# Optimization experiments

Measured on AMD Instinct MI355X. Metric: run time of the kernel, lower is better.

The kernel has to match this reference:

```python
import math
import jax, jax.numpy as jnp
import numpy as np

B, S, D = 8, 1024, 1024
H, DK = 16, 64
NUM_BUCKETS, MAX_DIST = 32, 128


def _relative_position_bucket(relative_position, num_buckets=NUM_BUCKETS, max_distance=MAX_DIST):
    # bidirectional=True branch of T5's bucket fn
    nb = num_buckets // 2
    n = -relative_position
    ret = (n < 0).astype(jnp.int32) * nb
    n = jnp.abs(n)
    max_exact = nb // 2
    is_small = n < max_exact
    n_safe = jnp.maximum(n, 1).astype(jnp.float32)
    val_if_large = max_exact + (
        jnp.log(n_safe / max_exact) / math.log(max_distance / max_exact) * (nb - max_exact)
    ).astype(jnp.int32)
    val_if_large = jnp.minimum(val_if_large, nb - 1)
    return ret + jnp.where(is_small, n, val_if_large)


def compute_bias(rel_emb, qlen, klen):
    ctx = jnp.arange(qlen)[:, None]
    mem = jnp.arange(klen)[None, :]
    rp_bucket = _relative_position_bucket(mem - ctx)          # [q, k]
    values = rel_emb[rp_bucket]                                # [q, k, H]
    return jnp.transpose(values, (2, 0, 1))[None]              # [1, H, q, k]


def setup_inputs() -> dict:
    key = jax.random.key(0)
    ks = jax.random.split(key, 6)
    sc = 0.02
    return {
        "x": jax.random.normal(ks[0], (B, S, D), jnp.float32),
        "Wq": jax.random.normal(ks[1], (D, H * DK), jnp.float32) * sc,
        "Wk": jax.random.normal(ks[2], (D, H * DK), jnp.float32) * sc,
        "Wv": jax.random.normal(ks[3], (D, H * DK), jnp.float32) * sc,
        "Wo": jax.random.normal(ks[4], (H * DK, D), jnp.float32) * sc,
        "rel_emb": jax.random.normal(ks[5], (NUM_BUCKETS, H), jnp.float32),
    }


def reference(x, Wq, Wk, Wv, Wo, rel_emb):
    bs, qlen, _ = x.shape

    def shape(t):  # [B, S, H*DK] -> [B, H, S, DK]
        return t.reshape(bs, -1, H, DK).transpose(0, 2, 1, 3)

    q = shape(x @ Wq)
    k = shape(x @ Wk)
    v = shape(x @ Wv)
    # T5 attention: NO 1/sqrt(dk) scaling
    scores = jnp.einsum("bhqd,bhkd->bhqk", q, k)
    position_bias = compute_bias(rel_emb, qlen, qlen)
    scores = scores + position_bias
    weights = jax.nn.softmax(scores.astype(jnp.float32), axis=-1).astype(scores.dtype)
    context = jnp.einsum("bhqk,bhkd->bhqd", weights, v)
    context = context.transpose(0, 2, 1, 3).reshape(bs, qlen, H * DK)
    return context @ Wo
```

## Files before the change

kernel.cpp:

```cpp
#include <hip/hip_runtime.h>
#include <stdint.h>

typedef uint16_t u16;
typedef uint32_t u32;
typedef __bf16 bf16;
typedef bf16 bf16x8 __attribute__((ext_vector_type(8)));
typedef bf16 bf16x4 __attribute__((ext_vector_type(4)));
typedef float f32x4 __attribute__((ext_vector_type(4)));
typedef u16 u16x4 __attribute__((ext_vector_type(4)));

#define MFMA(a, b, c) __builtin_amdgcn_mfma_f32_16x16x32_bf16((a), (b), (c), 0, 0, 0)

#define BATCH 8
#define SEQ 1024
#define DMODEL 1024
#define NH 16
#define DK 64
#define LOG2E 1.4426950408889634f

__device__ __forceinline__ u16 bfbits(float f) {
    bf16 h = (bf16)f;
    return __builtin_bit_cast(u16, h);
}

__device__ __forceinline__ float exp2_raw(float x) {
    float r;
    asm("v_exp_f32 %0, %1" : "=v"(r) : "v"(x));
    return r;
}

__device__ __forceinline__ void gload_lds16(const u16* g, u16* l) {
    __builtin_amdgcn_global_load_lds(
        (__attribute__((address_space(1))) void*)g,
        (__attribute__((address_space(3))) void*)l, 16, 0, 0);
}

__global__ __launch_bounds__(256) void prep_kernel(
        const float* __restrict__ x, const float* __restrict__ W0,
        const float* __restrict__ W1, const float* __restrict__ W2,
        const float* __restrict__ W3, const float* __restrict__ rel_emb,
        u16* __restrict__ xb, u16* __restrict__ T0, u16* __restrict__ T1,
        u16* __restrict__ T2, u16* __restrict__ T3, f32x4* __restrict__ F4) {
    __shared__ u16 Ts[64 * 72];
    const int bid = blockIdx.x, tid = threadIdx.x;
    if (bid < 8192) {
        size_t id = (size_t)bid * 256 + tid;
        f32x4 v = *(const f32x4*)(x + id * 4);
        bf16x4 o;
        o[0] = (bf16)v[0]; o[1] = (bf16)v[1]; o[2] = (bf16)v[2]; o[3] = (bf16)v[3];
        *(bf16x4*)(xb + id * 4) = o;
    } else if (bid < 9216) {
        const int t = bid - 8192;
        const int z = t >> 8, rem = t & 255;
        const float* W = (z == 0) ? W0 : (z == 1) ? W1 : (z == 2) ? W2 : W3;
        u16* T = (z == 0) ? T0 : (z == 1) ? T1 : (z == 2) ? T2 : T3;
        const int k0 = (rem >> 4) * 64, n0 = (rem & 15) * 64;
        const int r16 = tid >> 4, c0 = (tid & 15) * 4;
        #pragma unroll
        for (int rr = 0; rr < 4; rr++) {
            int r = rr * 16 + r16;
            f32x4 vv = *(const f32x4*)&W[(size_t)(k0 + r) * 1024 + n0 + c0];
            #pragma unroll
            for (int i = 0; i < 4; i++) Ts[(c0 + i) * 72 + r] = bfbits(vv[i]);
        }
        __syncthreads();
        int n = tid >> 2, seg = (tid & 3) * 16;
        *(bf16x8*)&T[(size_t)(n0 + n) * 1024 + k0 + seg] = *(const bf16x8*)&Ts[n * 72 + seg];
        *(bf16x8*)&T[(size_t)(n0 + n) * 1024 + k0 + seg + 8] =
            *(const bf16x8*)&Ts[n * 72 + seg + 8];
    } else {
        int id = (bid - 9216) * 256 + tid;
        if (id >= NH * 2047) return;
        int h = id / 2047, tt0 = id % 2047;
        f32x4 o;
        #pragma unroll
        for (int j = 0; j < 4; j++) {
            int tt = tt0 + j;
            float val = 0.f;
            if (tt <= 2046) {
                int rel = tt - 1023;
                int n = -rel;
                int b = 0;
                if (n < 0) { b = 16; n = -n; }
                int v;
                if (n < 8) {
                    v = n;
                } else {
                    int e = 31 - __clz(n);
                    int f = 2 * e + ((unsigned)(n * n) >= (1u << (2 * e + 1)) ? 1 : 0);
                    v = min(2 + f, 15);
                }
                val = LOG2E * rel_emb[(b + v) * NH + h];
            }
            o[j] = val;
        }
        F4[(size_t)h * 2047 + tt0] = o;
    }
}

__global__ __launch_bounds__(256) void gemm_qkv_kernel(
        const u16* __restrict__ xb,
        const u16* __restrict__ Wqt, const u16* __restrict__ Wkt, const u16* __restrict__ Wvt,
        u16* __restrict__ qb, u16* __restrict__ kb, u16* __restrict__ vb) {
    __shared__ u16 As[8192];
    __shared__ u16 Bs[8192];
    const int z = blockIdx.y >> 3;
    const u16* Bt = (z == 0) ? Wqt : (z == 1) ? Wkt : Wvt;
    const int m0 = blockIdx.x * 128, n0 = (blockIdx.y & 7) * 128;
    const int tid = threadIdx.x, w = tid >> 6, lane = tid & 63;
    const int quad = lane >> 4, l16 = lane & 15;
    const int rw = w >> 1, cw = w & 1;
    const int srow = lane >> 2, sseg = lane & 3;

    f32x4 acc[4][4];
    #pragma unroll
    for (int i = 0; i < 4; i++)
        #pragma unroll
        for (int j = 0; j < 4; j++) acc[i][j] = (f32x4){0.f, 0.f, 0.f, 0.f};

    for (int kk = 0; kk < 1024; kk += 64) {
        __syncthreads();
        #pragma unroll
        for (int p = 0; p < 2; p++) {
            #pragma unroll
            for (int r = 0; r < 2; r++) {
                int base = r * 64 + w * 16;
                int row = base + srow;
                gload_lds16(&xb[(size_t)(m0 + row) * 1024 + kk + p * 32 + sseg * 8],
                            &As[p * 4096 + base * 32]);
                gload_lds16(&Bt[(size_t)(n0 + row) * 1024 + kk + p * 32 + sseg * 8],
                            &Bs[p * 4096 + base * 32]);
            }
        }
        __syncthreads();
        #pragma unroll
        for (int p = 0; p < 2; p++) {
            bf16x8 af[4], bfr[4];
            #pragma unroll
            for (int mt = 0; mt < 4; mt++)
                af[mt] = *(const bf16x8*)&As[p * 4096 + (rw * 64 + mt * 16 + l16) * 32 + quad * 8];
            #pragma unroll
            for (int nt = 0; nt < 4; nt++)
                bfr[nt] = *(const bf16x8*)&Bs[p * 4096 + (cw * 64 + nt * 16 + l16) * 32 + quad * 8];
            #pragma unroll
            for (int mt = 0; mt < 4; mt++)
                #pragma unroll
                for (int nt = 0; nt < 4; nt++)
                    acc[mt][nt] = MFMA(af[mt], bfr[nt], acc[mt][nt]);
        }
    }

    #pragma unroll
    for (int mt = 0; mt < 4; mt++) {
        int gmBase = m0 + rw * 64 + mt * 16 + quad * 4;
        #pragma unroll
        for (int nt = 0; nt < 4; nt++) {
            int gn = n0 + cw * 64 + nt * 16 + l16;
            int h = gn >> 6, dk = gn & 63;
            if (z == 2) {
                int b_ = gmBase >> 10, s0 = gmBase & 1023;
                u16x4 pk = { bfbits(acc[mt][nt][0]), bfbits(acc[mt][nt][1]),
                             bfbits(acc[mt][nt][2]), bfbits(acc[mt][nt][3]) };
                *(u16x4*)&vb[(((size_t)b_ * NH + h) * DK + dk) * SEQ + s0] = pk;
            } else {
                u16* o = z ? kb : qb;
                #pragma unroll
                for (int r = 0; r < 4; r++) {
                    int gm = gmBase + r;
                    int b_ = gm >> 10, s = gm & 1023;
                    float sv = acc[mt][nt][r];
                    if (z == 0) sv *= LOG2E;
                    o[(((size_t)b_ * NH + h) * SEQ + s) * DK + dk] = bfbits(sv);
                }
            }
        }
    }
}

__global__ __launch_bounds__(256) void gemm_out_kernel(
        const u16* __restrict__ ctx, const u16* __restrict__ Wot, float* __restrict__ out) {
    __shared__ u16 As[8192];
    __shared__ u16 Bs[8192];
    const int m0 = blockIdx.x * 128, n0 = blockIdx.y * 128;
    const int tid = threadIdx.x, w = tid >> 6, lane = tid & 63;
    const int quad = lane >> 4, l16 = lane & 15;
    const int rw = w >> 1, cw = w & 1;
    const int srow = lane >> 2, sseg = lane & 3;

    f32x4 acc[4][4];
    #pragma unroll
    for (int i = 0; i < 4; i++)
        #pragma unroll
        for (int j = 0; j < 4; j++) acc[i][j] = (f32x4){0.f, 0.f, 0.f, 0.f};

    for (int kk = 0; kk < 1024; kk += 64) {
        __syncthreads();
        #pragma unroll
        for (int p = 0; p < 2; p++) {
            #pragma unroll
            for (int r = 0; r < 2; r++) {
                int base = r * 64 + w * 16;
                int row = base + srow;
                gload_lds16(&ctx[(size_t)(m0 + row) * 1024 + kk + p * 32 + sseg * 8],
                            &As[p * 4096 + base * 32]);
                gload_lds16(&Wot[(size_t)(n0 + row) * 1024 + kk + p * 32 + sseg * 8],
                            &Bs[p * 4096 + base * 32]);
            }
        }
        __syncthreads();
        #pragma unroll
        for (int p = 0; p < 2; p++) {
            bf16x8 af[4], bfr[4];
            #pragma unroll
            for (int mt = 0; mt < 4; mt++)
                af[mt] = *(const bf16x8*)&As[p * 4096 + (rw * 64 + mt * 16 + l16) * 32 + quad * 8];
            #pragma unroll
            for (int nt = 0; nt < 4; nt++)
                bfr[nt] = *(const bf16x8*)&Bs[p * 4096 + (cw * 64 + nt * 16 + l16) * 32 + quad * 8];
            #pragma unroll
            for (int mt = 0; mt < 4; mt++)
                #pragma unroll
                for (int nt = 0; nt < 4; nt++)
                    acc[mt][nt] = MFMA(af[mt], bfr[nt], acc[mt][nt]);
        }
    }

    #pragma unroll
    for (int mt = 0; mt < 4; mt++) {
        int gmBase = m0 + rw * 64 + mt * 16 + quad * 4;
        #pragma unroll
        for (int nt = 0; nt < 4; nt++) {
            int gn = n0 + cw * 64 + nt * 16 + l16;
            #pragma unroll
            for (int r = 0; r < 4; r++)
                out[(size_t)(gmBase + r) * 1024 + gn] = acc[mt][nt][r];
        }
    }
}

__global__ __launch_bounds__(256, 2) void attn_kernel(
        const u16* __restrict__ qb, const u16* __restrict__ kb,
        const u16* __restrict__ vb, const f32x4* __restrict__ F4,
        u16* __restrict__ ctx) {
    __shared__ u16 Kt[2][64 * 72];
    __shared__ u16 Vt[2][64 * 72];
    __shared__ u16 Pt[4][64 * 40];
    const int bh = blockIdx.x;
    const int h = bh & (NH - 1), b_ = bh >> 4;
    const int tid = threadIdx.x, w = tid >> 6, lane = tid & 63;
    const int quad = lane >> 4, l16 = lane & 15;
    const int q0 = blockIdx.y * 256 + w * 64;

    const f32x4* F4h = F4 + (size_t)h * 2047;
    const float cL = F4h[0][0];
    const float cR = F4h[2046][0];

    bf16x8 bq[4][2];
    #pragma unroll
    for (int mt = 0; mt < 4; mt++) {
        const u16* qrow = qb + ((size_t)bh * SEQ + q0 + mt * 16 + l16) * DK;
        bq[mt][0] = *(const bf16x8*)(qrow + quad * 8);
        bq[mt][1] = *(const bf16x8*)(qrow + 32 + quad * 8);
    }

    float l_[4] = {0.f, 0.f, 0.f, 0.f};
    f32x4 oacc[4][4];
    #pragma unroll
    for (int mt = 0; mt < 4; mt++)
        #pragma unroll
        for (int dt = 0; dt < 4; dt++) oacc[mt][dt] = (f32x4){0.f, 0.f, 0.f, 0.f};

    const int srow = tid >> 3, sseg = tid & 7;

    const u16* kbase_p = kb + (size_t)bh * SEQ * DK;
    const u16* vbase_p = vb + (size_t)bh * DK * SEQ;

    bf16x8 kr0, kr1, vr0, vr1;
    #define LOAD_TILE(nb)                                                        \
        kr0 = *(const bf16x8*)&kbase_p[(size_t)((nb) + srow) * DK + sseg * 8];   \
        kr1 = *(const bf16x8*)&kbase_p[(size_t)((nb) + srow + 32) * DK + sseg * 8]; \
        vr0 = *(const bf16x8*)&vbase_p[(size_t)srow * SEQ + (nb) + sseg * 8];    \
        vr1 = *(const bf16x8*)&vbase_p[(size_t)(srow + 32) * SEQ + (nb) + sseg * 8];
    #define WRITE_TILE(bi)                                                       \
        *(bf16x8*)&Kt[bi][srow * 72 + sseg * 8] = kr0;                           \
        *(bf16x8*)&Kt[bi][(srow + 32) * 72 + sseg * 8] = kr1;                    \
        *(bf16x8*)&Vt[bi][srow * 72 + sseg * 8] = vr0;                           \
        *(bf16x8*)&Vt[bi][(srow + 32) * 72 + sseg * 8] = vr1;

    LOAD_TILE(0)
    WRITE_TILE(0)
    LOAD_TILE(64)
    __syncthreads();

    for (int kt = 0; kt < 16; kt++) {
        const int kbase = kt * 64;
        const int cur = kt & 1;
        if (kt < 15) { WRITE_TILE(cur ^ 1) }
        if (kt < 14) { LOAD_TILE(kbase + 128) }

        f32x4 sc[4][4];
        if (kbase <= q0 - 154 || kbase >= q0 + 154) {
            const float cc = (kbase < q0) ? cL : cR;
            #pragma unroll
            for (int mt = 0; mt < 4; mt++)
                #pragma unroll
                for (int nt = 0; nt < 4; nt++)
                    sc[mt][nt] = (f32x4){cc, cc, cc, cc};
        } else {
            #pragma unroll
            for (int mt = 0; mt < 4; mt++)
                #pragma unroll
                for (int nt = 0; nt < 4; nt++) {
                    int t0 = (kbase + nt * 16 + quad * 4) - (q0 + mt * 16 + l16) + 1023;
                    sc[mt][nt] = F4h[t0];
                }
        }

        __builtin_amdgcn_s_setprio(1);
        #pragma unroll
        for (int nt = 0; nt < 4; nt++) {
            bf16x8 ak0 = *(const bf16x8*)&Kt[cur][(nt * 16 + l16) * 72 + quad * 8];
            bf16x8 ak1 = *(const bf16x8*)&Kt[cur][(nt * 16 + l16) * 72 + 32 + quad * 8];
            #pragma unroll
            for (int mt = 0; mt < 4; mt++) {
                sc[mt][nt] = MFMA(ak0, bq[mt][0], sc[mt][nt]);
                sc[mt][nt] = MFMA(ak1, bq[mt][1], sc[mt][nt]);
            }
        }
        __builtin_amdgcn_s_setprio(0);

        #pragma unroll
        for (int c = 0; c < 2; c++) {
            #pragma unroll
            for (int mt = 0; mt < 4; mt++) {
                #pragma unroll
                for (int i = 0; i < 2; i++) {
                    int nt = 2 * c + i;
                    float p0 = exp2_raw(sc[mt][nt][0]);
                    float p1 = exp2_raw(sc[mt][nt][1]);
                    float p2 = exp2_raw(sc[mt][nt][2]);
                    float p3 = exp2_raw(sc[mt][nt][3]);
                    l_[mt] += (p0 + p1) + (p2 + p3);
                    bf16x4 pk;
                    pk[0] = (bf16)p0; pk[1] = (bf16)p1;
                    pk[2] = (bf16)p2; pk[3] = (bf16)p3;
                    *(bf16x4*)&Pt[w][(mt * 16 + l16) * 40 + i * 16 + quad * 4] = pk;
                }
            }
            bf16x8 bp[4];
            #pragma unroll
            for (int mt = 0; mt < 4; mt++)
                bp[mt] = *(const bf16x8*)&Pt[w][(mt * 16 + l16) * 40 + quad * 8];
            __builtin_amdgcn_s_setprio(1);
            #pragma unroll
            for (int dt = 0; dt < 4; dt++) {
                bf16x8 av = *(const bf16x8*)&Vt[cur][(dt * 16 + l16) * 72 + c * 32 + quad * 8];
                #pragma unroll
                for (int mt = 0; mt < 4; mt++)
                    oacc[mt][dt] = MFMA(av, bp[mt], oacc[mt][dt]);
            }
            __builtin_amdgcn_s_setprio(0);
        }
        __syncthreads();
    }
    #undef LOAD_TILE
    #undef WRITE_TILE

    #pragma unroll
    for (int mt = 0; mt < 4; mt++) {
        float l = l_[mt];
        l += __shfl_xor(l, 16, 64);
        l += __shfl_xor(l, 32, 64);
        float inv = 1.f / l;
        int gq = q0 + mt * 16 + l16;
        #pragma unroll
        for (int dt = 0; dt < 4; dt++) {
            u16x4 pk = { bfbits(oacc[mt][dt][0] * inv), bfbits(oacc[mt][dt][1] * inv),
                         bfbits(oacc[mt][dt][2] * inv), bfbits(oacc[mt][dt][3] * inv) };
            *(u16x4*)&ctx[((size_t)b_ * SEQ + gq) * DMODEL + h * DK + dt * 16 + quad * 4] = pk;
        }
    }
}

extern "C" void kernel_launch(void* const* d_in, const int* in_sizes, int n_in,
                              void* d_out, int out_size, void* d_ws, size_t ws_size,
                              hipStream_t stream) {
    const float* x   = (const float*)d_in[0];
    const float* Wq  = (const float*)d_in[1];
    const float* Wk  = (const float*)d_in[2];
    const float* Wv  = (const float*)d_in[3];
    const float* Wo  = (const float*)d_in[4];
    const float* rel = (const float*)d_in[5];
    float* out = (float*)d_out;

    char* p = (char*)d_ws;
    u16* xb  = (u16*)p; p += (size_t)BATCH * SEQ * DMODEL * 2;
    u16* Wqt = (u16*)p; p += (size_t)DMODEL * DMODEL * 2;
    u16* Wkt = (u16*)p; p += (size_t)DMODEL * DMODEL * 2;
    u16* Wvt = (u16*)p; p += (size_t)DMODEL * DMODEL * 2;
    u16* Wot = (u16*)p; p += (size_t)DMODEL * DMODEL * 2;
    u16* qb  = (u16*)p; p += (size_t)BATCH * NH * SEQ * DK * 2;
    u16* kb  = (u16*)p; p += (size_t)BATCH * NH * SEQ * DK * 2;
    u16* vb  = (u16*)p; p += (size_t)BATCH * NH * SEQ * DK * 2;
    u16* ctx = (u16*)p; p += (size_t)BATCH * SEQ * DMODEL * 2;
    f32x4* F4 = (f32x4*)p; p += (size_t)NH * 2047 * 16;

    prep_kernel<<<9344, 256, 0, stream>>>(x, Wq, Wk, Wv, Wo, rel,
                                          xb, Wqt, Wkt, Wvt, Wot, F4);

    gemm_qkv_kernel<<<dim3(64, 24), 256, 0, stream>>>(xb, Wqt, Wkt, Wvt, qb, kb, vb);

    attn_kernel<<<dim3(128, 4), 256, 0, stream>>>(qb, kb, vb, F4, ctx);

    gemm_out_kernel<<<dim3(64, 8), 256, 0, stream>>>(ctx, Wot, out);
}
```

Baseline: 236.7 us.

## Stage K/V via direct global-to-LDS loads with XOR swizzle and 512-thread blocks

Replaces the register-staged K/V tile loads with direct global-to-LDS loads (gload_lds16) into an XOR-swizzled, unpadded LDS layout. Each block now has 8 waves covering 512 query rows, so each K/V tile loaded is shared by twice as many queries. The goal is to cut register pressure and VGPR round-trips and halve K/V global traffic per query. The cost is larger blocks that may lower occupancy, and it relies on the async LDS writes finishing before the single barrier per iteration.

```diff
diff --git a/kernel.cpp b/kernel.cpp
--- a/kernel.cpp
+++ b/kernel.cpp
@@ -238,18 +238,18 @@
     }
 }
 
-__global__ __launch_bounds__(256, 2) void attn_kernel(
+__global__ __launch_bounds__(512, 2) void attn_kernel(
         const u16* __restrict__ qb, const u16* __restrict__ kb,
         const u16* __restrict__ vb, const f32x4* __restrict__ F4,
         u16* __restrict__ ctx) {
-    __shared__ u16 Kt[2][64 * 72];
-    __shared__ u16 Vt[2][64 * 72];
-    __shared__ u16 Pt[4][64 * 40];
+    __shared__ u16 Kt[2][64 * 64];
+    __shared__ u16 Vt[2][64 * 64];
+    __shared__ u16 Pt[8][64 * 40];
     const int bh = blockIdx.x;
     const int h = bh & (NH - 1), b_ = bh >> 4;
     const int tid = threadIdx.x, w = tid >> 6, lane = tid & 63;
     const int quad = lane >> 4, l16 = lane & 15;
-    const int q0 = blockIdx.y * 256 + w * 64;
+    const int q0 = blockIdx.y * 512 + w * 64;
 
     const f32x4* F4h = F4 + (size_t)h * 2047;
     const float cL = F4h[0][0];
@@ -270,33 +270,24 @@
         #pragma unroll
         for (int dt = 0; dt < 4; dt++) oacc[mt][dt] = (f32x4){0.f, 0.f, 0.f, 0.f};
 
-    const int srow = tid >> 3, sseg = tid & 7;
-
     const u16* kbase_p = kb + (size_t)bh * SEQ * DK;
     const u16* vbase_p = vb + (size_t)bh * DK * SEQ;
 
-    bf16x8 kr0, kr1, vr0, vr1;
-    #define LOAD_TILE(nb)                                                        \
-        kr0 = *(const bf16x8*)&kbase_p[(size_t)((nb) + srow) * DK + sseg * 8];   \
-        kr1 = *(const bf16x8*)&kbase_p[(size_t)((nb) + srow + 32) * DK + sseg * 8]; \
-        vr0 = *(const bf16x8*)&vbase_p[(size_t)srow * SEQ + (nb) + sseg * 8];    \
-        vr1 = *(const bf16x8*)&vbase_p[(size_t)(srow + 32) * SEQ + (nb) + sseg * 8];
-    #define WRITE_TILE(bi)                                                       \
-        *(bf16x8*)&Kt[bi][srow * 72 + sseg * 8] = kr0;                           \
-        *(bf16x8*)&Kt[bi][(srow + 32) * 72 + sseg * 8] = kr1;                    \
-        *(bf16x8*)&Vt[bi][srow * 72 + sseg * 8] = vr0;                           \
-        *(bf16x8*)&Vt[bi][(srow + 32) * 72 + sseg * 8] = vr1;
-
-    LOAD_TILE(0)
-    WRITE_TILE(0)
-    LOAD_TILE(64)
+    const int rl = lane >> 3, slot = lane & 7;
+    const int strow = w * 8 + rl, sseg = (slot ^ rl) * 8;
+    #define STAGE(bi, kb0)                                                       \
+        gload_lds16(&kbase_p[(size_t)((kb0) + strow) * DK + sseg],               \
+                    &Kt[bi][w * 512]);                                           \
+        gload_lds16(&vbase_p[(size_t)strow * SEQ + (kb0) + sseg],                \
+                    &Vt[bi][w * 512]);
+
+    STAGE(0, 0)
     __syncthreads();
 
     for (int kt = 0; kt < 16; kt++) {
         const int kbase = kt * 64;
         const int cur = kt & 1;
-        if (kt < 15) { WRITE_TILE(cur ^ 1) }
-        if (kt < 14) { LOAD_TILE(kbase + 128) }
+        if (kt < 15) { STAGE(cur ^ 1, kbase + 64) }
 
         f32x4 sc[4][4];
         if (kbase <= q0 - 154 || kbase >= q0 + 154) {
@@ -319,8 +310,10 @@
         __builtin_amdgcn_s_setprio(1);
         #pragma unroll
         for (int nt = 0; nt < 4; nt++) {
-            bf16x8 ak0 = *(const bf16x8*)&Kt[cur][(nt * 16 + l16) * 72 + quad * 8];
-            bf16x8 ak1 = *(const bf16x8*)&Kt[cur][(nt * 16 + l16) * 72 + 32 + quad * 8];
+            const int rk = nt * 16 + l16, swk = rk & 7;
+            const u16* ktp = &Kt[cur][rk * 64];
+            bf16x8 ak0 = *(const bf16x8*)&ktp[(quad ^ swk) * 8];
+            bf16x8 ak1 = *(const bf16x8*)&ktp[((quad + 4) ^ swk) * 8];
             #pragma unroll
             for (int mt = 0; mt < 4; mt++) {
                 sc[mt][nt] = MFMA(ak0, bq[mt][0], sc[mt][nt]);
@@ -354,17 +347,17 @@
             __builtin_amdgcn_s_setprio(1);
             #pragma unroll
             for (int dt = 0; dt < 4; dt++) {
-                bf16x8 av = *(const bf16x8*)&Vt[cur][(dt * 16 + l16) * 72 + c * 32 + quad * 8];
+                const int rv = dt * 16 + l16;
+                bf16x8 av = *(const bf16x8*)&Vt[cur][rv * 64 + (((c * 4 + quad) ^ (rv & 7)) * 8)];
                 #pragma unroll
                 for (int mt = 0; mt < 4; mt++)
                     oacc[mt][dt] = MFMA(av, bp[mt], oacc[mt][dt]);
             }
             __builtin_amdgcn_s_setprio(0);
         }
-        __syncthreads();
-    }
-    #undef LOAD_TILE
-    #undef WRITE_TILE
+        if (kt < 15) __syncthreads();
+    }
+    #undef STAGE
 
     #pragma unroll
     for (int mt = 0; mt < 4; mt++) {
@@ -410,7 +403,7 @@
 
     gemm_qkv_kernel<<<dim3(64, 24), 256, 0, stream>>>(xb, Wqt, Wkt, Wvt, qb, kb, vb);
 
-    attn_kernel<<<dim3(128, 4), 256, 0, stream>>>(qb, kb, vb, F4, ctx);
+    attn_kernel<<<dim3(128, 2), 512, 0, stream>>>(qb, kb, vb, F4, ctx);
 
     gemm_out_kernel<<<dim3(64, 8), 256, 0, stream>>>(ctx, Wot, out);
 }
```

Result: no change. 234.6 us (-0.9%).
